# Kernel optimization log

Hardware: AMD Instinct MI355X
Metric: run time of the kernel (lower is better)

## Reference

```python
import jax, jax.numpy as jnp
import numpy as np

HIDDEN = 2048
INTER = 5632
TOKENS = 8192


def setup_inputs() -> dict:
    key = jax.random.key(0)
    k1, k2, k3 = jax.random.split(key, 3)
    x = jax.random.normal(k1, (TOKENS, HIDDEN), dtype=jnp.float32)
    # gate_up_weight = [gate_weight | up_weight], shape [hidden, 2*intermediate]
    gate_up_weight = jax.random.normal(k2, (HIDDEN, 2 * INTER), dtype=jnp.float32) * (1.0 / np.sqrt(HIDDEN))
    down_weight = jax.random.normal(k3, (INTER, HIDDEN), dtype=jnp.float32) * (1.0 / np.sqrt(INTER))
    return {"x": x, "gate_up_weight": gate_up_weight, "down_weight": down_weight}


def reference(x, gate_up_weight, down_weight):
    # Fused SwiGLU expert MLP: SiLU(x @ Wg) * (x @ Wu) @ Wd
    inter = gate_up_weight.shape[1] // 2
    gate_up = jnp.matmul(x, gate_up_weight)          # [T, 2*I]
    gate, up = gate_up[:, :inter], gate_up[:, inter:]
    hidden = jax.nn.silu(gate) * up                   # [T, I]
    out = jnp.matmul(hidden, down_weight)             # [T, H]
    return out.astype(x.dtype)
```

## Files before the change

### kernel.cpp

```cpp
#include <hip/hip_runtime.h>
#include <stdint.h>

typedef unsigned short u16;
typedef __attribute__((ext_vector_type(8))) __bf16 bf16x8;
typedef __attribute__((ext_vector_type(8))) u16 u16x8;
typedef __attribute__((ext_vector_type(4))) float f32x4;

#define HID 2048
#define INTER 5632
#define TOKENS 8192

__device__ __forceinline__ u16 f2bf(float f) {
  uint32_t u = __builtin_bit_cast(uint32_t, f);
  u += 0x7fffu + ((u >> 16) & 1u);
  return (u16)(u >> 16);
}

__device__ __forceinline__ void gld_lds16(const u16* g, u16* l) {
  __builtin_amdgcn_global_load_lds(
      (const __attribute__((address_space(1))) unsigned int*)g,
      (__attribute__((address_space(3))) unsigned int*)l, 16, 0, 0);
}


__global__ void k_cvt_x(const float* __restrict__ in, u16* __restrict__ out) {
  size_t i = (size_t)blockIdx.x * 256 + threadIdx.x;
  const float4* p = (const float4*)(in + i * 8);
  float4 a = p[0], b = p[1];
  u16x8 o;
  o[0] = f2bf(a.x); o[1] = f2bf(a.y); o[2] = f2bf(a.z); o[3] = f2bf(a.w);
  o[4] = f2bf(b.x); o[5] = f2bf(b.y); o[6] = f2bf(b.z); o[7] = f2bf(b.w);
  *(u16x8*)(out + i * 8) = o;
}

__global__ __launch_bounds__(256) void k_transpose64(
    const float* __restrict__ in, u16* __restrict__ out, int R, int C) {
  __shared__ float t[64][65];
  int c0 = blockIdx.x * 64, r0 = blockIdx.y * 64;
  int tid = threadIdx.x;
  int tx = tid & 15, ry = tid >> 4;
#pragma unroll
  for (int r = 0; r < 4; ++r) {
    int row = r * 16 + ry;
    float4 v = *(const float4*)(in + (size_t)(r0 + row) * C + c0 + tx * 4);
    t[row][tx * 4 + 0] = v.x; t[row][tx * 4 + 1] = v.y;
    t[row][tx * 4 + 2] = v.z; t[row][tx * 4 + 3] = v.w;
  }
  __syncthreads();
  int cc = tid >> 2, seg = tid & 3;
#pragma unroll
  for (int h = 0; h < 2; ++h) {
    int rr0 = seg * 16 + h * 8;
    u16x8 o;
#pragma unroll
    for (int j = 0; j < 8; ++j) o[j] = f2bf(t[rr0 + j][cc]);
    *(u16x8*)(out + (size_t)(c0 + cc) * R + r0 + rr0) = o;
  }
}

__global__ __launch_bounds__(256, 2) void k_gemm1(
    const u16* __restrict__ xb, const u16* __restrict__ w1t,
    u16* __restrict__ hid) {
  __shared__ __align__(16) u16 sA[128 * 64];
  __shared__ __align__(16) u16 sG[64 * 64];
  __shared__ __align__(16) u16 sU[64 * 64];
  const int K = HID;
  int brow = blockIdx.y * 128, bcol = blockIdx.x * 64;
  int tid = threadIdx.x, lane = tid & 63, wid = tid >> 6;
  int wm = wid >> 1, wn = wid & 1;
  f32x4 accg[4][2] = {}, accu[4][2] = {};
  const u16* gA = xb + (size_t)brow * K;
  const u16* gG = w1t + (size_t)bcol * K;
  const u16* gU = w1t + (size_t)(bcol + INTER) * K;
  int tr = tid >> 3;
  int tc = (tid & 7) * 8;
  int cb = lane & 15, kb = (lane >> 4) * 8;

  for (int kt = 0; kt < K / 64; ++kt) {
    int k0 = kt * 64;
#pragma unroll
    for (int r = 0; r < 4; ++r) {
      int row = r * 32 + tr;
      gld_lds16(gA + (size_t)row * K + k0 + tc, &sA[row * 64 + tc]);
    }
#pragma unroll
    for (int r = 0; r < 2; ++r) {
      int row = r * 32 + tr;
      gld_lds16(gG + (size_t)row * K + k0 + tc, &sG[row * 64 + tc]);
      gld_lds16(gU + (size_t)row * K + k0 + tc, &sU[row * 64 + tc]);
    }
    __syncthreads();
#pragma unroll
    for (int ks = 0; ks < 2; ++ks) {
      int kk = ks * 32 + kb;
      bf16x8 af[4];
#pragma unroll
      for (int m = 0; m < 4; ++m)
        af[m] = *(const bf16x8*)&sA[(wm * 64 + m * 16 + cb) * 64 + kk];
#pragma unroll
      for (int n = 0; n < 2; ++n) {
        bf16x8 bg = *(const bf16x8*)&sG[(wn * 32 + n * 16 + cb) * 64 + kk];
        bf16x8 bu = *(const bf16x8*)&sU[(wn * 32 + n * 16 + cb) * 64 + kk];
#pragma unroll
        for (int m = 0; m < 4; ++m) {
          accg[m][n] = __builtin_amdgcn_mfma_f32_16x16x32_bf16(af[m], bg, accg[m][n], 0, 0, 0);
          accu[m][n] = __builtin_amdgcn_mfma_f32_16x16x32_bf16(af[m], bu, accu[m][n], 0, 0, 0);
        }
      }
    }
    __syncthreads();
  }
  int rb = (lane >> 4) * 4;
#pragma unroll
  for (int m = 0; m < 4; ++m)
#pragma unroll
    for (int n = 0; n < 2; ++n) {
      int col = bcol + wn * 32 + n * 16 + cb;
#pragma unroll
      for (int i = 0; i < 4; ++i) {
        int row = brow + wm * 64 + m * 16 + rb + i;
        float g = accg[m][n][i], u = accu[m][n][i];
        float h = g / (1.0f + __expf(-g)) * u;
        hid[(size_t)row * INTER + col] = f2bf(h);
      }
    }
}


#define STAGE(dst, srcBase, stride, kt)                                        \
  do {                                                                         \
    const int _k0 = (kt) * 64;                                                 \
    _Pragma("unroll") for (int _r = 0; _r < 2; ++_r) {                         \
      const int _prow = _r * 64 + wid * 8 + srow;                              \
      const u16* _src = (srcBase) + (size_t)_prow * (stride) + _k0 +           \
                        ((schunk ^ (_prow & 7)) * 8);                          \
      gld_lds16(_src, (dst) + _prow * 64 + schunk * 8);                        \
    }                                                                          \
  } while (0)

#define LOAD_A(bufp, mh)                                                       \
  do {                                                                         \
    _Pragma("unroll") for (int _jj = 0; _jj < 4; ++_jj) {                      \
      const int _row = ((mh)*4 + _jj) * 32 + wm * 16 + cb;                     \
      _Pragma("unroll") for (int _ks = 0; _ks < 2; ++_ks) {                    \
        const int _ch = (_ks * 4 + hi) ^ (cb & 7);                             \
        aF[_jj][_ks] = *(const bf16x8*)((bufp) + _row * 64 + _ch * 8);         \
      }                                                                        \
    }                                                                          \
  } while (0)

#define LOAD_B(bufp, nh)                                                       \
  do {                                                                         \
    _Pragma("unroll") for (int _nn = 0; _nn < 2; ++_nn) {                      \
      const int _row = ((nh)*2 + _nn) * 64 + wn * 16 + cb;                     \
      _Pragma("unroll") for (int _ks = 0; _ks < 2; ++_ks) {                    \
        const int _ch = (_ks * 4 + hi) ^ (cb & 7);                             \
        bF[_nn][_ks] = *(const bf16x8*)((bufp) + _row * 64 + _ch * 8);         \
      }                                                                        \
    }                                                                          \
  } while (0)

#define MMA_Q(mh, nh)                                                          \
  do {                                                                         \
    _Pragma("unroll") for (int _ks = 0; _ks < 2; ++_ks)                        \
    _Pragma("unroll") for (int _jj = 0; _jj < 4; ++_jj)                        \
    _Pragma("unroll") for (int _nn = 0; _nn < 2; ++_nn)                        \
      acc[(mh)*4 + _jj][(nh)*2 + _nn] =                                        \
          __builtin_amdgcn_mfma_f32_16x16x32_bf16(                             \
              aF[_jj][_ks], bF[_nn][_ks], acc[(mh)*4 + _jj][(nh)*2 + _nn],     \
              0, 0, 0);                                                        \
  } while (0)

__global__ __launch_bounds__(512, 2) void k_gemm2_v3(
    const u16* __restrict__ hid, const u16* __restrict__ w2t,
    float* __restrict__ out) {
  __shared__ __align__(16) u16 sA[2][256 * 64];
  __shared__ __align__(16) u16 sB[2][256 * 64];
  const int NT = INTER / 64;
  const int brow = blockIdx.y * 256, bcol = blockIdx.x * 256;

  const int tid = threadIdx.x, lane = tid & 63, wid = tid >> 6;
  const int wm = wid >> 2, wn = wid & 3;
  const int cb = lane & 15, hi = lane >> 4;
  const int srow = lane >> 3, schunk = lane & 7;

  f32x4 acc[8][4] = {};
  bf16x8 aF[4][2], bF[2][2];

  const u16* gA0 = hid + (size_t)brow * INTER;
  const u16* gA1 = gA0 + (size_t)128 * INTER;
  const u16* gB0 = w2t + (size_t)bcol * INTER;
  const u16* gB1 = w2t + (size_t)(bcol + 128) * INTER;

  STAGE(sA[0], gA0, INTER, 0);
  STAGE(sB[0], gB0, INTER, 0);
  STAGE(sA[0] + 128 * 64, gA1, INTER, 0);
  STAGE(sB[0] + 128 * 64, gB1, INTER, 0);
  __builtin_amdgcn_sched_barrier(0);
  asm volatile("s_waitcnt vmcnt(4)" ::: "memory");
  __builtin_amdgcn_s_barrier();

  for (int t = 0; t < NT; ++t) {
    u16* bufA = sA[t & 1];
    u16* bufB = sB[t & 1];
    u16* nA = sA[(t & 1) ^ 1];
    u16* nB = sB[(t & 1) ^ 1];
    const bool hn = (t + 1 < NT);

    if (hn) { STAGE(nA, gA0, INTER, t + 1); STAGE(nB, gB0, INTER, t + 1); }
    LOAD_A(bufA, 0); LOAD_B(bufB, 0);
    __builtin_amdgcn_s_barrier();
    __builtin_amdgcn_s_setprio(1); MMA_Q(0, 0); __builtin_amdgcn_s_setprio(0);
    __builtin_amdgcn_sched_barrier(0);
    if (hn) asm volatile("s_waitcnt vmcnt(4)" ::: "memory");
    else    asm volatile("s_waitcnt vmcnt(0)" ::: "memory");
    __builtin_amdgcn_s_barrier();

    if (hn) {
      STAGE(nA + 128 * 64, gA1, INTER, t + 1);
      STAGE(nB + 128 * 64, gB1, INTER, t + 1);
    }
    LOAD_A(bufA, 1);
    __builtin_amdgcn_s_barrier();
    __builtin_amdgcn_s_setprio(1); MMA_Q(1, 0); __builtin_amdgcn_s_setprio(0);
    __builtin_amdgcn_s_barrier();

    LOAD_B(bufB, 1);
    __builtin_amdgcn_s_barrier();
    __builtin_amdgcn_s_setprio(1); MMA_Q(1, 1); __builtin_amdgcn_s_setprio(0);
    __builtin_amdgcn_s_barrier();

    LOAD_A(bufA, 0);
    __builtin_amdgcn_s_barrier();
    __builtin_amdgcn_s_setprio(1); MMA_Q(0, 1); __builtin_amdgcn_s_setprio(0);
    __builtin_amdgcn_sched_barrier(0);
    if (hn) asm volatile("s_waitcnt vmcnt(4)" ::: "memory");
    __builtin_amdgcn_s_barrier();
  }

#pragma unroll
  for (int j = 0; j < 8; ++j)
#pragma unroll
    for (int n = 0; n < 4; ++n) {
      const int col = bcol + n * 64 + wn * 16 + cb;
#pragma unroll
      for (int i = 0; i < 4; ++i) {
        const int row = brow + j * 32 + wm * 16 + hi * 4 + i;
        out[(size_t)row * HID + col] = acc[j][n][i];
      }
    }
}


extern "C" void kernel_launch(void* const* d_in, const int* in_sizes, int n_in,
                              void* d_out, int out_size, void* d_ws, size_t ws_size,
                              hipStream_t stream) {
  const float* x  = (const float*)d_in[0];
  const float* w1 = (const float*)d_in[1];
  const float* w2 = (const float*)d_in[2];
  float* out = (float*)d_out;

  const size_t off_xb  = 0;
  const size_t off_w1t = 33554432;
  const size_t off_w2t = off_w1t + 46137344;
  const size_t off_hid = off_w2t + 23068672;
  const size_t need    = off_hid + 92274688;
  if (ws_size < need) return;

  char* ws = (char*)d_ws;
  u16* xb  = (u16*)(ws + off_xb);
  u16* w1t = (u16*)(ws + off_w1t);
  u16* w2t = (u16*)(ws + off_w2t);
  u16* hid = (u16*)(ws + off_hid);

  k_cvt_x<<<TOKENS * HID / 8 / 256, 256, 0, stream>>>(x, xb);
  k_transpose64<<<dim3((2 * INTER) / 64, HID / 64), 256, 0, stream>>>(w1, w1t, HID, 2 * INTER);
  k_transpose64<<<dim3(HID / 64, INTER / 64), 256, 0, stream>>>(w2, w2t, INTER, HID);

  k_gemm1<<<dim3(INTER / 64, TOKENS / 128), 256, 0, stream>>>(xb, w1t, hid);
  k_gemm2_v3<<<dim3(HID / 256, TOKENS / 256), 512, 0, stream>>>(hid, w2t, out);
}
```

Before: 831.0 us.

## Restructure gemm2 pipeline to prefetch half-tiles two iterations ahead

Rewrites the down-projection GEMM main loop so that global-to-LDS staging of A and B half-tiles is spread across the four MMA quadrants and issued up to two k-steps ahead, reusing each buffer as soon as its quadrant is consumed. The quadrant order changes so every half-tile's last use comes before it is overwritten, and the vmcnt wait depth increases. The goal is to keep more memory traffic in flight and hide load latency behind MFMA work. The cost is tighter buffer-reuse hazards that depend on correct barrier and waitcnt placement.

```diff
diff --git a/kernel.cpp b/kernel.cpp
--- a/kernel.cpp
+++ b/kernel.cpp
@@ -9,6 +9,7 @@
 #define HID 2048
 #define INTER 5632
 #define TOKENS 8192
+#define HALF (128 * 64)
 
 __device__ __forceinline__ u16 f2bf(float f) {
   uint32_t u = __builtin_bit_cast(uint32_t, f);
@@ -171,7 +172,7 @@
               0, 0, 0);                                                        \
   } while (0)
 
-__global__ __launch_bounds__(512, 2) void k_gemm2_v3(
+__global__ __launch_bounds__(512, 2) void k_gemm2_hk(
     const u16* __restrict__ hid, const u16* __restrict__ w2t,
     float* __restrict__ out) {
   __shared__ __align__(16) u16 sA[2][256 * 64];
@@ -194,47 +195,46 @@
 
   STAGE(sA[0], gA0, INTER, 0);
   STAGE(sB[0], gB0, INTER, 0);
-  STAGE(sA[0] + 128 * 64, gA1, INTER, 0);
-  STAGE(sB[0] + 128 * 64, gB1, INTER, 0);
+  STAGE(sA[0] + HALF, gA1, INTER, 0);
+  STAGE(sB[0] + HALF, gB1, INTER, 0);
+  STAGE(sA[1], gA0, INTER, 1);
+  STAGE(sB[1] + HALF, gB1, INTER, 1);
+  STAGE(sA[1] + HALF, gA1, INTER, 1);
   __builtin_amdgcn_sched_barrier(0);
-  asm volatile("s_waitcnt vmcnt(4)" ::: "memory");
+  asm volatile("s_waitcnt vmcnt(6)" ::: "memory");
   __builtin_amdgcn_s_barrier();
 
   for (int t = 0; t < NT; ++t) {
     u16* bufA = sA[t & 1];
     u16* bufB = sB[t & 1];
-    u16* nA = sA[(t & 1) ^ 1];
-    u16* nB = sB[(t & 1) ^ 1];
-    const bool hn = (t + 1 < NT);
-
-    if (hn) { STAGE(nA, gA0, INTER, t + 1); STAGE(nB, gB0, INTER, t + 1); }
+    u16* nbB = sB[(t & 1) ^ 1];
+    const bool s1 = (t + 1 < NT), s2 = (t + 2 < NT);
+
     LOAD_A(bufA, 0); LOAD_B(bufB, 0);
+    if (s1) STAGE(nbB, gB0, INTER, t + 1);
     __builtin_amdgcn_s_barrier();
     __builtin_amdgcn_s_setprio(1); MMA_Q(0, 0); __builtin_amdgcn_s_setprio(0);
+    __builtin_amdgcn_s_barrier();
+
+    LOAD_B(bufB, 1);
+    if (s2) STAGE(bufA, gA0, INTER, t + 2);
+    __builtin_amdgcn_s_barrier();
+    __builtin_amdgcn_s_setprio(1); MMA_Q(0, 1); __builtin_amdgcn_s_setprio(0);
+    __builtin_amdgcn_s_barrier();
+
+    LOAD_A(bufA, 1);
+    if (s2) STAGE(bufB + HALF, gB1, INTER, t + 2);
+    __builtin_amdgcn_s_barrier();
+    __builtin_amdgcn_s_setprio(1); MMA_Q(1, 1); __builtin_amdgcn_s_setprio(0);
+    __builtin_amdgcn_s_barrier();
+
+    LOAD_B(bufB, 0);
+    if (s2) STAGE(bufA + HALF, gA1, INTER, t + 2);
+    __builtin_amdgcn_s_barrier();
+    __builtin_amdgcn_s_setprio(1); MMA_Q(1, 0); __builtin_amdgcn_s_setprio(0);
     __builtin_amdgcn_sched_barrier(0);
-    if (hn) asm volatile("s_waitcnt vmcnt(4)" ::: "memory");
-    else    asm volatile("s_waitcnt vmcnt(0)" ::: "memory");
-    __builtin_amdgcn_s_barrier();
-
-    if (hn) {
-      STAGE(nA + 128 * 64, gA1, INTER, t + 1);
-      STAGE(nB + 128 * 64, gB1, INTER, t + 1);
-    }
-    LOAD_A(bufA, 1);
-    __builtin_amdgcn_s_barrier();
-    __builtin_amdgcn_s_setprio(1); MMA_Q(1, 0); __builtin_amdgcn_s_setprio(0);
-    __builtin_amdgcn_s_barrier();
-
-    LOAD_B(bufB, 1);
-    __builtin_amdgcn_s_barrier();
-    __builtin_amdgcn_s_setprio(1); MMA_Q(1, 1); __builtin_amdgcn_s_setprio(0);
-    __builtin_amdgcn_s_barrier();
-
-    LOAD_A(bufA, 0);
-    __builtin_amdgcn_s_barrier();
-    __builtin_amdgcn_s_setprio(1); MMA_Q(0, 1); __builtin_amdgcn_s_setprio(0);
-    __builtin_amdgcn_sched_barrier(0);
-    if (hn) asm volatile("s_waitcnt vmcnt(4)" ::: "memory");
+    if (s2)      asm volatile("s_waitcnt vmcnt(6)" ::: "memory");
+    else if (s1) asm volatile("s_waitcnt vmcnt(0)" ::: "memory");
     __builtin_amdgcn_s_barrier();
   }
 
@@ -278,5 +278,5 @@
   k_transpose64<<<dim3(HID / 64, INTER / 64), 256, 0, stream>>>(w2, w2t, INTER, HID);
 
   k_gemm1<<<dim3(INTER / 64, TOKENS / 128), 256, 0, stream>>>(xb, w1t, hid);
-  k_gemm2_v3<<<dim3(HID / 256, TOKENS / 256), 512, 0, stream>>>(hid, w2t, out);
-}
+  k_gemm2_hk<<<dim3(HID / 256, TOKENS / 256), 512, 0, stream>>>(hid, w2t, out);
+}
```

Result: faster. 808.8 us (-2.7%).
